# Kernel tuning notes

Measured on AMD Instinct MI355X. Metric: run time of the kernel, lower is better.

Reference implementation:

```python
import jax, jax.numpy as jnp
import numpy as np

NEG_SLOPE = 0.01  # torch nn.LeakyReLU default

N_NODES = 100000
N_EDGES = 1000000
D_FEAT = 64


def setup_inputs() -> dict:
    key = jax.random.key(0)
    ks = jax.random.split(key, 8)
    x = jax.random.normal(ks[0], (N_NODES, D_FEAT), dtype=jnp.float32)
    src = jax.random.randint(ks[1], (N_EDGES,), 0, N_NODES, dtype=jnp.int64 if jax.config.jax_enable_x64 else jnp.int32)
    dst = jax.random.randint(ks[2], (N_EDGES,), 0, N_NODES, dtype=jnp.int64 if jax.config.jax_enable_x64 else jnp.int32)
    s = 1.0 / np.sqrt(D_FEAT)
    W1 = jax.random.normal(ks[3], (D_FEAT, 64), dtype=jnp.float32) * s
    b1 = jnp.zeros((64,), dtype=jnp.float32)
    W2 = jax.random.normal(ks[4], (64, 64), dtype=jnp.float32) * s
    b2 = jnp.zeros((64,), dtype=jnp.float32)
    Wc = jax.random.normal(ks[5], (64, 2), dtype=jnp.float32) * s
    bc = jnp.zeros((2,), dtype=jnp.float32)
    return {"x": x, "src": src, "dst": dst, "W1": W1, "b1": b1,
            "W2": W2, "b2": b2, "Wc": Wc, "bc": bc}


def _graph_conv(x, src, dst, W, b, out_deg_isqrt, in_deg_isqrt, n_nodes):
    # DGL GraphConv, norm='both': h_v = ( sum_{u->v} x_u / sqrt(d_out(u)) ) / sqrt(d_in(v)) @ W + b
    # (in_feats <= out_feats here, so aggregate first then transform, matching DGL order)
    h = x * out_deg_isqrt[:, None]          # [N, d] scale by source out-degree
    msg = h[src]                            # [E, d] gather
    agg = jax.ops.segment_sum(msg, dst, num_segments=n_nodes)  # [N, d] scatter-add
    agg = agg * in_deg_isqrt[:, None]
    return agg @ W + b


def reference(x, src, dst, W1, b1, W2, b2, Wc, bc):
    n = x.shape[0]
    ones_e = jnp.ones(src.shape[0], dtype=x.dtype)
    out_deg = jnp.clip(jax.ops.segment_sum(ones_e, src, num_segments=n), 1.0)
    in_deg = jnp.clip(jax.ops.segment_sum(ones_e, dst, num_segments=n), 1.0)
    out_isqrt = out_deg ** -0.5
    in_isqrt = in_deg ** -0.5

    h = _graph_conv(x, src, dst, W1, b1, out_isqrt, in_isqrt, n)
    h = jax.nn.leaky_relu(h, NEG_SLOPE)
    h = _graph_conv(h, src, dst, W2, b2, out_isqrt, in_isqrt, n)
    h = jax.nn.leaky_relu(h, NEG_SLOPE)
    return h @ Wc + bc  # prediction=True -> linear classifier
```

## Files before the change

kernel.cpp:

```cpp
#include <hip/hip_runtime.h>


typedef __attribute__((ext_vector_type(8))) short short8;
typedef __attribute__((ext_vector_type(4))) float f32x4;

#define NPB 256
#define BSH 9
#define BW  512

__device__ __forceinline__ float b2f(unsigned short u) {
    return __uint_as_float(((unsigned int)u) << 16);
}
__device__ __forceinline__ unsigned short f2b(float f) {
    unsigned int i = __float_as_uint(f);
    unsigned int r = (i + 0x7FFFu + ((i >> 16) & 1u)) >> 16;
    return (unsigned short)r;
}

__global__ __launch_bounds__(256) void count_kernel(
    const int* __restrict__ src, const int* __restrict__ dst,
    int* __restrict__ cntD, int* __restrict__ cntS, int e, int chunk) {
    __shared__ int hD[256], hS[256];
    int t = threadIdx.x, pb = blockIdx.x;
    hD[t] = 0; hS[t] = 0;
    __syncthreads();
    int e0 = pb * chunk, e1 = min(e, e0 + chunk);
    for (int i = e0 + t; i < e1; i += 256) {
        atomicAdd(&hD[dst[i] >> BSH], 1);
        atomicAdd(&hS[src[i] >> BSH], 1);
    }
    __syncthreads();
    cntD[t * NPB + pb] = hD[t];
    cntS[t * NPB + pb] = hS[t];
}

__global__ __launch_bounds__(1024) void scanmat_kernel(int* __restrict__ cntD,
                                                       int* __restrict__ cntS) {
    int* a = (blockIdx.x == 0) ? cntD : cntS;
    __shared__ int s[1024];
    int t = threadIdx.x;
    int base = t * 64;
    int sum = 0;
    for (int j = 0; j < 64; j++) sum += a[base + j];
    s[t] = sum;
    __syncthreads();
    for (int d = 1; d < 1024; d <<= 1) {
        int x = (t >= d) ? s[t - d] : 0;
        __syncthreads();
        s[t] += x;
        __syncthreads();
    }
    int run = s[t] - sum;
    for (int j = 0; j < 64; j++) {
        int v = a[base + j];
        a[base + j] = run;
        run += v;
    }
}

__global__ __launch_bounds__(256) void part_kernel(
    const int* __restrict__ src, const int* __restrict__ dst,
    const int* __restrict__ cntD, const int* __restrict__ cntS,
    unsigned int* __restrict__ ebuf, unsigned short* __restrict__ sbuf,
    int e, int chunk) {
    __shared__ int cD[256], cS[256];
    int t = threadIdx.x, pb = blockIdx.x;
    cD[t] = cntD[t * NPB + pb];
    cS[t] = cntS[t * NPB + pb];
    __syncthreads();
    int e0 = pb * chunk, e1 = min(e, e0 + chunk);
    for (int i = e0 + t; i < e1; i += 256) {
        int s_ = src[i], d_ = dst[i];
        int pd = atomicAdd(&cD[d_ >> BSH], 1);
        ebuf[pd] = ((unsigned int)s_ << BSH) | (unsigned int)(d_ & (BW - 1));
        int ps_ = atomicAdd(&cS[s_ >> BSH], 1);
        sbuf[ps_] = (unsigned short)(s_ & (BW - 1));
    }
}

__global__ __launch_bounds__(256) void bucket_kernel(
    const unsigned int* __restrict__ ebuf, const unsigned short* __restrict__ sbuf,
    const int* __restrict__ cntD, const int* __restrict__ cntS,
    const float4* __restrict__ x4,
    int* __restrict__ row, float* __restrict__ ii, float* __restrict__ oi,
    int* __restrict__ csr, ushort4* __restrict__ xb, int n, int e) {
    __shared__ int cnt[BW], cur[BW], ocnt[BW], ps[256];
    __shared__ float ol[BW];
    int t = threadIdx.x, b = blockIdx.x;
    int v0 = b << BSH;
    int eb0 = cntD[b * NPB], eb1 = cntD[(b + 1) * NPB];
    int sb0 = cntS[b * NPB], sb1 = cntS[(b + 1) * NPB];
    cnt[t] = 0; cnt[t + 256] = 0;
    ocnt[t] = 0; ocnt[t + 256] = 0;
    __syncthreads();
    for (int i = eb0 + t; i < eb1; i += 256)
        atomicAdd(&cnt[ebuf[i] & (BW - 1)], 1);
    for (int i = sb0 + t; i < sb1; i += 256)
        atomicAdd(&ocnt[sbuf[i]], 1);
    __syncthreads();
    int c0 = cnt[2 * t], c1 = cnt[2 * t + 1];
    int pair = c0 + c1;
    ps[t] = pair;
    __syncthreads();
    for (int d = 1; d < 256; d <<= 1) {
        int x = (t >= d) ? ps[t - d] : 0;
        __syncthreads();
        ps[t] += x;
        __syncthreads();
    }
    int excl = ps[t] - pair;
    cur[2 * t] = excl;
    cur[2 * t + 1] = excl + c0;
    int v = v0 + 2 * t;
    if (v < n) {
        row[v] = eb0 + excl;
        ii[v] = rsqrtf((float)max(c0, 1));
    }
    if (v + 1 < n) {
        row[v + 1] = eb0 + excl + c0;
        ii[v + 1] = rsqrtf((float)max(c1, 1));
    }
    if (b == 0 && t == 0) row[n] = e;
    for (int j = t; j < BW; j += 256) {
        float o = rsqrtf((float)max(ocnt[j], 1));
        ol[j] = o;
        int vv = v0 + j;
        if (vv < n) oi[vv] = o;
    }
    __syncthreads();
    for (int i = eb0 + t; i < eb1; i += 256) {
        unsigned int p = ebuf[i];
        int r = atomicAdd(&cur[p & (BW - 1)], 1);
        csr[eb0 + r] = (int)(p >> BSH);
    }
    int nloc = min(BW, n - v0);
    for (int i = t; i < nloc * 16; i += 256) {
        int vl = i >> 4, q = i & 15;
        float s = ol[vl];
        float4 val = x4[(size_t)(v0 + vl) * 16 + q];
        xb[(size_t)(v0 + vl) * 16 + q] =
            make_ushort4(f2b(val.x * s), f2b(val.y * s), f2b(val.z * s), f2b(val.w * s));
    }
}

__global__ __launch_bounds__(256) void agg_kernel(
    const ushort4* __restrict__ featb, const int* __restrict__ row,
    const int* __restrict__ csr, float4* __restrict__ out4,
    int n, int nwaves) {
    int lane = threadIdx.x & 63;
    int q = lane >> 4, s = lane & 15;
    int wid = blockIdx.x * (blockDim.x >> 6) + (threadIdx.x >> 6);
    int ngroups = (n + 3) >> 2;

    for (int g = wid; g < ngroups; g += nwaves) {
        int v = (g << 2) + q;
        bool valid = v < n;
        int base = 0, cnt = 0;
        if (valid) { base = row[v]; cnt = row[v + 1] - base; }
        float4 a = make_float4(0.f, 0.f, 0.f, 0.f);
        int j = 0;
        for (; j + 7 < cnt; j += 8) {
            int u[8];
#pragma unroll
            for (int k = 0; k < 8; k++) u[k] = csr[base + j + k];
#pragma unroll
            for (int k = 0; k < 8; k++) {
                ushort4 f = featb[(size_t)u[k] * 16 + s];
                a.x += b2f(f.x); a.y += b2f(f.y); a.z += b2f(f.z); a.w += b2f(f.w);
            }
        }
        for (; j + 3 < cnt; j += 4) {
            int u[4];
#pragma unroll
            for (int k = 0; k < 4; k++) u[k] = csr[base + j + k];
#pragma unroll
            for (int k = 0; k < 4; k++) {
                ushort4 f = featb[(size_t)u[k] * 16 + s];
                a.x += b2f(f.x); a.y += b2f(f.y); a.z += b2f(f.z); a.w += b2f(f.w);
            }
        }
        for (; j < cnt; j++) {
            ushort4 f = featb[(size_t)csr[base + j] * 16 + s];
            a.x += b2f(f.x); a.y += b2f(f.y); a.z += b2f(f.z); a.w += b2f(f.w);
        }
        if (valid) out4[(size_t)v * 16 + s] = a;
    }
}

template <bool FINAL>
__global__ __launch_bounds__(256) void gemm_kernel(
    const float* __restrict__ agg, const float* __restrict__ ii,
    const float* __restrict__ oi,
    const float* __restrict__ W, const float* __restrict__ bias,
    const float* __restrict__ Wc, const float* __restrict__ bcl,
    void* __restrict__ out, int n, int nwaves) {
    int lane = threadIdx.x & 63;
    int m15 = lane & 15, quad = lane >> 4;
    int wid = blockIdx.x * (blockDim.x >> 6) + (threadIdx.x >> 6);
    int ngroups = (n + 15) >> 4;

    short8 bf[4][2];
#pragma unroll
    for (int nt = 0; nt < 4; nt++)
#pragma unroll
        for (int kk = 0; kk < 2; kk++)
#pragma unroll
            for (int j = 0; j < 8; j++)
                bf[nt][kk][j] = (short)f2b(W[(kk * 32 + quad * 8 + j) * 64 + nt * 16 + m15]);

    float bias_r[4];
#pragma unroll
    for (int nt = 0; nt < 4; nt++) bias_r[nt] = bias[nt * 16 + m15];

    float wc_r[4][2];
    float bc0 = 0.f, bc1 = 0.f;
    if constexpr (FINAL) {
#pragma unroll
        for (int nt = 0; nt < 4; nt++) {
            wc_r[nt][0] = Wc[(nt * 16 + m15) * 2];
            wc_r[nt][1] = Wc[(nt * 16 + m15) * 2 + 1];
        }
        bc0 = bcl[0];
        bc1 = bcl[1];
    }

    for (int g = wid; g < ngroups; g += nwaves) {
        int rbase = g << 4;
        int rm = min(rbase + m15, n - 1);
        float iiv = ii[rm];

        short8 af[2];
#pragma unroll
        for (int kk = 0; kk < 2; kk++) {
            const float4* p = (const float4*)(agg + (size_t)rm * 64 + kk * 32 + quad * 8);
            float4 x0 = p[0], x1 = p[1];
            af[kk][0] = (short)f2b(x0.x * iiv);
            af[kk][1] = (short)f2b(x0.y * iiv);
            af[kk][2] = (short)f2b(x0.z * iiv);
            af[kk][3] = (short)f2b(x0.w * iiv);
            af[kk][4] = (short)f2b(x1.x * iiv);
            af[kk][5] = (short)f2b(x1.y * iiv);
            af[kk][6] = (short)f2b(x1.z * iiv);
            af[kk][7] = (short)f2b(x1.w * iiv);
        }

        f32x4 acc[4];
#pragma unroll
        for (int nt = 0; nt < 4; nt++) {
            f32x4 z = {0.f, 0.f, 0.f, 0.f};
            z = __builtin_amdgcn_mfma_f32_16x16x32_bf16(af[0], bf[nt][0], z, 0, 0, 0);
            z = __builtin_amdgcn_mfma_f32_16x16x32_bf16(af[1], bf[nt][1], z, 0, 0, 0);
            acc[nt] = z;
        }

        if constexpr (!FINAL) {
#pragma unroll
            for (int r = 0; r < 4; r++) {
                int vr = rbase + quad * 4 + r;
                float os = (vr < n) ? oi[vr] : 0.f;
#pragma unroll
                for (int nt = 0; nt < 4; nt++) {
                    float o = acc[nt][r] + bias_r[nt];
                    o = (o > 0.f) ? o : 0.01f * o;
                    if (vr < n)
                        ((unsigned short*)out)[(size_t)vr * 64 + nt * 16 + m15] = f2b(o * os);
                }
            }
        } else {
#pragma unroll
            for (int r = 0; r < 4; r++) {
                float p0 = 0.f, p1 = 0.f;
#pragma unroll
                for (int nt = 0; nt < 4; nt++) {
                    float o = acc[nt][r] + bias_r[nt];
                    o = (o > 0.f) ? o : 0.01f * o;
                    p0 = fmaf(o, wc_r[nt][0], p0);
                    p1 = fmaf(o, wc_r[nt][1], p1);
                }
#pragma unroll
                for (int off = 1; off < 16; off <<= 1) {
                    p0 += __shfl_xor(p0, off);
                    p1 += __shfl_xor(p1, off);
                }
                int vr = rbase + quad * 4 + r;
                if (m15 == 0 && vr < n)
                    ((float2*)out)[vr] = make_float2(p0 + bc0, p1 + bc1);
            }
        }
    }
}

extern "C" void kernel_launch(void* const* d_in, const int* in_sizes, int n_in,
                              void* d_out, int out_size, void* d_ws, size_t ws_size,
                              hipStream_t stream) {
    const float* x  = (const float*)d_in[0];
    const int* src  = (const int*)d_in[1];
    const int* dst  = (const int*)d_in[2];
    const float* W1 = (const float*)d_in[3];
    const float* b1 = (const float*)d_in[4];
    const float* W2 = (const float*)d_in[5];
    const float* b2 = (const float*)d_in[6];
    const float* Wc = (const float*)d_in[7];
    const float* bc = (const float*)d_in[8];
    int n = in_sizes[0] / 64;
    int e = in_sizes[1];
    int total = n * 64;
    int nbuck = (n + BW - 1) >> BSH;

    char* ws = (char*)d_ws;
    size_t off = 0;
    auto take = [&](size_t bytes) -> char* {
        char* p = ws + off;
        off = (off + bytes + 255) & ~(size_t)255;
        return p;
    };
    int* cntD = (int*)take(256 * NPB * 4);
    int* cntS = (int*)take(256 * NPB * 4);
    unsigned int* ebuf = (unsigned int*)take((size_t)e * 4);
    unsigned short* sbuf = (unsigned short*)take((size_t)e * 2);
    int* row  = (int*)take((size_t)(n + 1) * 4);
    int* csr  = (int*)take((size_t)e * 4);
    float* oi = (float*)take((size_t)n * 4);
    float* ii = (float*)take((size_t)n * 4);
    unsigned short* xb  = (unsigned short*)take((size_t)total * 2);
    unsigned short* h1b = (unsigned short*)take((size_t)total * 2);
    float* aggbuf = (float*)take((size_t)total * 4);

    const int tb = 256;
    int chunk = (e + NPB - 1) / NPB;

    count_kernel<<<NPB, tb, 0, stream>>>(src, dst, cntD, cntS, e, chunk);
    scanmat_kernel<<<2, 1024, 0, stream>>>(cntD, cntS);
    part_kernel<<<NPB, tb, 0, stream>>>(src, dst, cntD, cntS, ebuf, sbuf, e, chunk);
    bucket_kernel<<<nbuck, tb, 0, stream>>>(ebuf, sbuf, cntD, cntS, (const float4*)x,
                                            row, ii, oi, csr, (ushort4*)xb, n, e);

    const int ablocks = 2048;
    const int awaves = ablocks * (tb / 64);
    const int gblocks = 512;
    const int gwaves = gblocks * (tb / 64);

    agg_kernel<<<ablocks, tb, 0, stream>>>((const ushort4*)xb, row, csr,
                                           (float4*)aggbuf, n, awaves);
    gemm_kernel<false><<<gblocks, tb, 0, stream>>>(aggbuf, ii, oi, W1, b1,
                                                   nullptr, nullptr, h1b, n, gwaves);
    agg_kernel<<<ablocks, tb, 0, stream>>>((const ushort4*)h1b, row, csr,
                                           (float4*)aggbuf, n, awaves);
    gemm_kernel<true><<<gblocks, tb, 0, stream>>>(aggbuf, ii, nullptr, W2, b2,
                                                  Wc, bc, d_out, n, gwaves);
}
```

Baseline: 232.4 us.

## Fuse neighbor aggregation and MFMA transform into one per-tile layer kernel

Each GCN layer becomes a single kernel. A block aggregates 128 destination nodes into padded LDS, synchronises, then runs the bf16 MFMA transform with bias, LeakyReLU and scaling straight from shared memory. This removes the fp32 aggregation buffer round-trip through global memory and two kernel launches. The cost is grid-stride balancing traded for fixed tiles of 782 blocks, roughly 35 KB of LDS per block, and W fragment setup repeated in every block.

```diff
diff --git a/kernel.cpp b/kernel.cpp
--- a/kernel.cpp
+++ b/kernel.cpp
@@ -7,6 +7,9 @@
 #define NPB 256
 #define BSH 9
 #define BW  512
+#define TSH 7
+#define TW  128
+#define STR 68
 
 __device__ __forceinline__ float b2f(unsigned short u) {
     return __uint_as_float(((unsigned int)u) << 16);
@@ -143,17 +146,48 @@
     }
 }
 
-__global__ __launch_bounds__(256) void agg_kernel(
+template <bool FINAL>
+__global__ __launch_bounds__(256) void layer_kernel(
     const ushort4* __restrict__ featb, const int* __restrict__ row,
-    const int* __restrict__ csr, float4* __restrict__ out4,
-    int n, int nwaves) {
-    int lane = threadIdx.x & 63;
+    const int* __restrict__ csr, const float* __restrict__ ii,
+    const float* __restrict__ oi,
+    const float* __restrict__ W, const float* __restrict__ bias,
+    const float* __restrict__ Wc, const float* __restrict__ bcl,
+    void* __restrict__ out, int n) {
+    __shared__ float accL[TW * STR];
+    int tid = threadIdx.x;
+    int lane = tid & 63;
+    int w = tid >> 6;
     int q = lane >> 4, s = lane & 15;
-    int wid = blockIdx.x * (blockDim.x >> 6) + (threadIdx.x >> 6);
-    int ngroups = (n + 3) >> 2;
-
-    for (int g = wid; g < ngroups; g += nwaves) {
-        int v = (g << 2) + q;
+    int m15 = s, quad = q;
+    int v0 = blockIdx.x << TSH;
+
+    short8 bf[4][2];
+#pragma unroll
+    for (int nt = 0; nt < 4; nt++)
+#pragma unroll
+        for (int kk = 0; kk < 2; kk++)
+#pragma unroll
+            for (int j = 0; j < 8; j++)
+                bf[nt][kk][j] = (short)f2b(W[(kk * 32 + quad * 8 + j) * 64 + nt * 16 + m15]);
+    float bias_r[4];
+#pragma unroll
+    for (int nt = 0; nt < 4; nt++) bias_r[nt] = bias[nt * 16 + m15];
+    float wc_r[4][2];
+    float bc0 = 0.f, bc1 = 0.f;
+    if constexpr (FINAL) {
+#pragma unroll
+        for (int nt = 0; nt < 4; nt++) {
+            wc_r[nt][0] = Wc[(nt * 16 + m15) * 2];
+            wc_r[nt][1] = Wc[(nt * 16 + m15) * 2 + 1];
+        }
+        bc0 = bcl[0];
+        bc1 = bcl[1];
+    }
+
+    for (int gl = w; gl < TW / 4; gl += 4) {
+        int vL = gl * 4 + q;
+        int v = v0 + vL;
         bool valid = v < n;
         int base = 0, cnt = 0;
         if (valid) { base = row[v]; cnt = row[v + 1] - base; }
@@ -183,56 +217,19 @@
             ushort4 f = featb[(size_t)csr[base + j] * 16 + s];
             a.x += b2f(f.x); a.y += b2f(f.y); a.z += b2f(f.z); a.w += b2f(f.w);
         }
-        if (valid) out4[(size_t)v * 16 + s] = a;
-    }
-}
-
-template <bool FINAL>
-__global__ __launch_bounds__(256) void gemm_kernel(
-    const float* __restrict__ agg, const float* __restrict__ ii,
-    const float* __restrict__ oi,
-    const float* __restrict__ W, const float* __restrict__ bias,
-    const float* __restrict__ Wc, const float* __restrict__ bcl,
-    void* __restrict__ out, int n, int nwaves) {
-    int lane = threadIdx.x & 63;
-    int m15 = lane & 15, quad = lane >> 4;
-    int wid = blockIdx.x * (blockDim.x >> 6) + (threadIdx.x >> 6);
-    int ngroups = (n + 15) >> 4;
-
-    short8 bf[4][2];
-#pragma unroll
-    for (int nt = 0; nt < 4; nt++)
-#pragma unroll
-        for (int kk = 0; kk < 2; kk++)
-#pragma unroll
-            for (int j = 0; j < 8; j++)
-                bf[nt][kk][j] = (short)f2b(W[(kk * 32 + quad * 8 + j) * 64 + nt * 16 + m15]);
-
-    float bias_r[4];
-#pragma unroll
-    for (int nt = 0; nt < 4; nt++) bias_r[nt] = bias[nt * 16 + m15];
-
-    float wc_r[4][2];
-    float bc0 = 0.f, bc1 = 0.f;
-    if constexpr (FINAL) {
-#pragma unroll
-        for (int nt = 0; nt < 4; nt++) {
-            wc_r[nt][0] = Wc[(nt * 16 + m15) * 2];
-            wc_r[nt][1] = Wc[(nt * 16 + m15) * 2 + 1];
-        }
-        bc0 = bcl[0];
-        bc1 = bcl[1];
-    }
-
-    for (int g = wid; g < ngroups; g += nwaves) {
-        int rbase = g << 4;
-        int rm = min(rbase + m15, n - 1);
-        float iiv = ii[rm];
+        *(float4*)&accL[vL * STR + s * 4] = a;
+    }
+    __syncthreads();
+
+    for (int t8 = w; t8 < TW / 16; t8 += 4) {
+        int rl = t8 * 16;
+        int rg = v0 + rl + m15;
+        float iiv = ii[min(rg, n - 1)];
 
         short8 af[2];
 #pragma unroll
         for (int kk = 0; kk < 2; kk++) {
-            const float4* p = (const float4*)(agg + (size_t)rm * 64 + kk * 32 + quad * 8);
+            const float4* p = (const float4*)&accL[(rl + m15) * STR + kk * 32 + quad * 8];
             float4 x0 = p[0], x1 = p[1];
             af[kk][0] = (short)f2b(x0.x * iiv);
             af[kk][1] = (short)f2b(x0.y * iiv);
@@ -256,7 +253,7 @@
         if constexpr (!FINAL) {
 #pragma unroll
             for (int r = 0; r < 4; r++) {
-                int vr = rbase + quad * 4 + r;
+                int vr = v0 + rl + quad * 4 + r;
                 float os = (vr < n) ? oi[vr] : 0.f;
 #pragma unroll
                 for (int nt = 0; nt < 4; nt++) {
@@ -282,7 +279,7 @@
                     p0 += __shfl_xor(p0, off);
                     p1 += __shfl_xor(p1, off);
                 }
-                int vr = rbase + quad * 4 + r;
+                int vr = v0 + rl + quad * 4 + r;
                 if (m15 == 0 && vr < n)
                     ((float2*)out)[vr] = make_float2(p0 + bc0, p1 + bc1);
             }
@@ -306,6 +303,7 @@
     int e = in_sizes[1];
     int total = n * 64;
     int nbuck = (n + BW - 1) >> BSH;
+    int ntile = (n + TW - 1) >> TSH;
 
     char* ws = (char*)d_ws;
     size_t off = 0;
@@ -324,7 +322,6 @@
     float* ii = (float*)take((size_t)n * 4);
     unsigned short* xb  = (unsigned short*)take((size_t)total * 2);
     unsigned short* h1b = (unsigned short*)take((size_t)total * 2);
-    float* aggbuf = (float*)take((size_t)total * 4);
 
     const int tb = 256;
     int chunk = (e + NPB - 1) / NPB;
@@ -335,17 +332,8 @@
     bucket_kernel<<<nbuck, tb, 0, stream>>>(ebuf, sbuf, cntD, cntS, (const float4*)x,
                                             row, ii, oi, csr, (ushort4*)xb, n, e);
 
-    const int ablocks = 2048;
-    const int awaves = ablocks * (tb / 64);
-    const int gblocks = 512;
-    const int gwaves = gblocks * (tb / 64);
-
-    agg_kernel<<<ablocks, tb, 0, stream>>>((const ushort4*)xb, row, csr,
-                                           (float4*)aggbuf, n, awaves);
-    gemm_kernel<false><<<gblocks, tb, 0, stream>>>(aggbuf, ii, oi, W1, b1,
-                                                   nullptr, nullptr, h1b, n, gwaves);
-    agg_kernel<<<ablocks, tb, 0, stream>>>((const ushort4*)h1b, row, csr,
-                                           (float4*)aggbuf, n, awaves);
-    gemm_kernel<true><<<gblocks, tb, 0, stream>>>(aggbuf, ii, nullptr, W2, b2,
-                                                  Wc, bc, d_out, n, gwaves);
-}
+    layer_kernel<false><<<ntile, tb, 0, stream>>>((const ushort4*)xb, row, csr, ii, oi,
+                                                  W1, b1, nullptr, nullptr, h1b, n);
+    layer_kernel<true><<<ntile, tb, 0, stream>>>((const ushort4*)h1b, row, csr, ii, oi,
+                                                 W2, b2, Wc, bc, d_out, n);
+}
```

Measured after the change: 303.5 us. 30.6% more time.

## Sort nodes by in-degree within buckets to balance aggregation waves

Applied to the files above, without the earlier changes.

The bucket kernel now counting-sorts the nodes of each 512-node bucket by in-degree (capped at 63) and writes a permutation. The aggregation kernel processes nodes in permuted order, so the four nodes sharing a wave have similar degrees and fewer lanes sit idle waiting on the longest neighbour list. This costs an extra indirection read per node, scattered output writes, and a serial 64-entry scan on one thread per bucket.

```diff
diff --git a/kernel.cpp b/kernel.cpp
--- a/kernel.cpp
+++ b/kernel.cpp
@@ -83,15 +83,19 @@
     const int* __restrict__ cntD, const int* __restrict__ cntS,
     const float4* __restrict__ x4,
     int* __restrict__ row, float* __restrict__ ii, float* __restrict__ oi,
-    int* __restrict__ csr, ushort4* __restrict__ xb, int n, int e) {
+    int* __restrict__ csr, ushort4* __restrict__ xb, int* __restrict__ perm,
+    int n, int e) {
     __shared__ int cnt[BW], cur[BW], ocnt[BW], ps[256];
     __shared__ float ol[BW];
+    __shared__ int dh[64];
     int t = threadIdx.x, b = blockIdx.x;
     int v0 = b << BSH;
     int eb0 = cntD[b * NPB], eb1 = cntD[(b + 1) * NPB];
     int sb0 = cntS[b * NPB], sb1 = cntS[(b + 1) * NPB];
+    int nloc = min(BW, n - v0);
     cnt[t] = 0; cnt[t + 256] = 0;
     ocnt[t] = 0; ocnt[t + 256] = 0;
+    if (t < 64) dh[t] = 0;
     __syncthreads();
     for (int i = eb0 + t; i < eb1; i += 256)
         atomicAdd(&cnt[ebuf[i] & (BW - 1)], 1);
@@ -127,13 +131,23 @@
         int vv = v0 + j;
         if (vv < n) oi[vv] = o;
     }
-    __syncthreads();
+    for (int j = t; j < nloc; j += 256)
+        atomicAdd(&dh[min(cnt[j], 63)], 1);
+    __syncthreads();
+    if (t == 0) {
+        int acc = 0;
+        for (int d = 0; d < 64; d++) { int x = dh[d]; dh[d] = acc; acc += x; }
+    }
+    __syncthreads();
+    for (int j = t; j < nloc; j += 256) {
+        int pos = atomicAdd(&dh[min(cnt[j], 63)], 1);
+        perm[v0 + pos] = v0 + j;
+    }
     for (int i = eb0 + t; i < eb1; i += 256) {
         unsigned int p = ebuf[i];
         int r = atomicAdd(&cur[p & (BW - 1)], 1);
         csr[eb0 + r] = (int)(p >> BSH);
     }
-    int nloc = min(BW, n - v0);
     for (int i = t; i < nloc * 16; i += 256) {
         int vl = i >> 4, q = i & 15;
         float s = ol[vl];
@@ -145,8 +159,8 @@
 
 __global__ __launch_bounds__(256) void agg_kernel(
     const ushort4* __restrict__ featb, const int* __restrict__ row,
-    const int* __restrict__ csr, float4* __restrict__ out4,
-    int n, int nwaves) {
+    const int* __restrict__ csr, const int* __restrict__ perm,
+    float4* __restrict__ out4, int n, int nwaves) {
     int lane = threadIdx.x & 63;
     int q = lane >> 4, s = lane & 15;
     int wid = blockIdx.x * (blockDim.x >> 6) + (threadIdx.x >> 6);
@@ -155,8 +169,12 @@
     for (int g = wid; g < ngroups; g += nwaves) {
         int v = (g << 2) + q;
         bool valid = v < n;
-        int base = 0, cnt = 0;
-        if (valid) { base = row[v]; cnt = row[v + 1] - base; }
+        int pv = 0, base = 0, cnt = 0;
+        if (valid) {
+            pv = perm[v];
+            base = row[pv];
+            cnt = row[pv + 1] - base;
+        }
         float4 a = make_float4(0.f, 0.f, 0.f, 0.f);
         int j = 0;
         for (; j + 7 < cnt; j += 8) {
@@ -183,7 +201,7 @@
             ushort4 f = featb[(size_t)csr[base + j] * 16 + s];
             a.x += b2f(f.x); a.y += b2f(f.y); a.z += b2f(f.z); a.w += b2f(f.w);
         }
-        if (valid) out4[(size_t)v * 16 + s] = a;
+        if (valid) out4[(size_t)pv * 16 + s] = a;
     }
 }
 
@@ -320,6 +338,7 @@
     unsigned short* sbuf = (unsigned short*)take((size_t)e * 2);
     int* row  = (int*)take((size_t)(n + 1) * 4);
     int* csr  = (int*)take((size_t)e * 4);
+    int* perm = (int*)take((size_t)n * 4);
     float* oi = (float*)take((size_t)n * 4);
     float* ii = (float*)take((size_t)n * 4);
     unsigned short* xb  = (unsigned short*)take((size_t)total * 2);
@@ -333,18 +352,18 @@
     scanmat_kernel<<<2, 1024, 0, stream>>>(cntD, cntS);
     part_kernel<<<NPB, tb, 0, stream>>>(src, dst, cntD, cntS, ebuf, sbuf, e, chunk);
     bucket_kernel<<<nbuck, tb, 0, stream>>>(ebuf, sbuf, cntD, cntS, (const float4*)x,
-                                            row, ii, oi, csr, (ushort4*)xb, n, e);
+                                            row, ii, oi, csr, (ushort4*)xb, perm, n, e);
 
     const int ablocks = 2048;
     const int awaves = ablocks * (tb / 64);
     const int gblocks = 512;
     const int gwaves = gblocks * (tb / 64);
 
-    agg_kernel<<<ablocks, tb, 0, stream>>>((const ushort4*)xb, row, csr,
+    agg_kernel<<<ablocks, tb, 0, stream>>>((const ushort4*)xb, row, csr, perm,
                                            (float4*)aggbuf, n, awaves);
     gemm_kernel<false><<<gblocks, tb, 0, stream>>>(aggbuf, ii, oi, W1, b1,
                                                    nullptr, nullptr, h1b, n, gwaves);
-    agg_kernel<<<ablocks, tb, 0, stream>>>((const ushort4*)h1b, row, csr,
+    agg_kernel<<<ablocks, tb, 0, stream>>>((const ushort4*)h1b, row, csr, perm,
                                            (float4*)aggbuf, n, awaves);
     gemm_kernel<true><<<gblocks, tb, 0, stream>>>(aggbuf, ii, nullptr, W2, b2,
                                                   Wc, bc, d_out, n, gwaves);
```

Result: slower. 243.7 us (+4.9%).

## Store aggregation output as scaled bf16 and widen gather to 16-byte loads

Applied to the files above, without the earlier changes.

The aggregation kernel now applies the in-degree scale and writes its result as bf16, so the intermediate buffer is half the size and the GEMM loads ready-made MFMA operands directly. The gather changes from 8-byte to 16-byte loads, with 8 lanes per node and 8 nodes per wave, and the 8-wide unrolled inner loop is removed. The aim is to cut intermediate write and read traffic and the number of gather transactions. In exchange there are fewer lanes per node row, more accumulator registers per lane, and a shallower unroll that may expose less memory-level parallelism.

```diff
diff --git a/kernel.cpp b/kernel.cpp
--- a/kernel.cpp
+++ b/kernel.cpp
@@ -144,52 +144,54 @@
 }
 
 __global__ __launch_bounds__(256) void agg_kernel(
-    const ushort4* __restrict__ featb, const int* __restrict__ row,
-    const int* __restrict__ csr, float4* __restrict__ out4,
-    int n, int nwaves) {
+    const short8* __restrict__ featb, const int* __restrict__ row,
+    const int* __restrict__ csr, const float* __restrict__ ii,
+    short8* __restrict__ outb, int n, int nwaves) {
     int lane = threadIdx.x & 63;
-    int q = lane >> 4, s = lane & 15;
+    int o = lane >> 3, s = lane & 7;
     int wid = blockIdx.x * (blockDim.x >> 6) + (threadIdx.x >> 6);
-    int ngroups = (n + 3) >> 2;
+    int ngroups = (n + 7) >> 3;
 
     for (int g = wid; g < ngroups; g += nwaves) {
-        int v = (g << 2) + q;
+        int v = (g << 3) + o;
         bool valid = v < n;
         int base = 0, cnt = 0;
         if (valid) { base = row[v]; cnt = row[v + 1] - base; }
-        float4 a = make_float4(0.f, 0.f, 0.f, 0.f);
+        float a[8];
+#pragma unroll
+        for (int k = 0; k < 8; k++) a[k] = 0.f;
         int j = 0;
-        for (; j + 7 < cnt; j += 8) {
-            int u[8];
-#pragma unroll
-            for (int k = 0; k < 8; k++) u[k] = csr[base + j + k];
-#pragma unroll
-            for (int k = 0; k < 8; k++) {
-                ushort4 f = featb[(size_t)u[k] * 16 + s];
-                a.x += b2f(f.x); a.y += b2f(f.y); a.z += b2f(f.z); a.w += b2f(f.w);
-            }
-        }
         for (; j + 3 < cnt; j += 4) {
             int u[4];
 #pragma unroll
             for (int k = 0; k < 4; k++) u[k] = csr[base + j + k];
 #pragma unroll
             for (int k = 0; k < 4; k++) {
-                ushort4 f = featb[(size_t)u[k] * 16 + s];
-                a.x += b2f(f.x); a.y += b2f(f.y); a.z += b2f(f.z); a.w += b2f(f.w);
+                short8 f = featb[(size_t)u[k] * 8 + s];
+#pragma unroll
+                for (int m = 0; m < 8; m++)
+                    a[m] += b2f((unsigned short)f[m]);
             }
         }
         for (; j < cnt; j++) {
-            ushort4 f = featb[(size_t)csr[base + j] * 16 + s];
-            a.x += b2f(f.x); a.y += b2f(f.y); a.z += b2f(f.z); a.w += b2f(f.w);
-        }
-        if (valid) out4[(size_t)v * 16 + s] = a;
+            short8 f = featb[(size_t)csr[base + j] * 8 + s];
+#pragma unroll
+            for (int m = 0; m < 8; m++)
+                a[m] += b2f((unsigned short)f[m]);
+        }
+        if (valid) {
+            float iiv = ii[v];
+            short8 r;
+#pragma unroll
+            for (int m = 0; m < 8; m++) r[m] = (short)f2b(a[m] * iiv);
+            outb[(size_t)v * 8 + s] = r;
+        }
     }
 }
 
 template <bool FINAL>
 __global__ __launch_bounds__(256) void gemm_kernel(
-    const float* __restrict__ agg, const float* __restrict__ ii,
+    const unsigned short* __restrict__ aggb,
     const float* __restrict__ oi,
     const float* __restrict__ W, const float* __restrict__ bias,
     const float* __restrict__ Wc, const float* __restrict__ bcl,
@@ -227,29 +229,17 @@
     for (int g = wid; g < ngroups; g += nwaves) {
         int rbase = g << 4;
         int rm = min(rbase + m15, n - 1);
-        float iiv = ii[rm];
-
-        short8 af[2];
-#pragma unroll
-        for (int kk = 0; kk < 2; kk++) {
-            const float4* p = (const float4*)(agg + (size_t)rm * 64 + kk * 32 + quad * 8);
-            float4 x0 = p[0], x1 = p[1];
-            af[kk][0] = (short)f2b(x0.x * iiv);
-            af[kk][1] = (short)f2b(x0.y * iiv);
-            af[kk][2] = (short)f2b(x0.z * iiv);
-            af[kk][3] = (short)f2b(x0.w * iiv);
-            af[kk][4] = (short)f2b(x1.x * iiv);
-            af[kk][5] = (short)f2b(x1.y * iiv);
-            af[kk][6] = (short)f2b(x1.z * iiv);
-            af[kk][7] = (short)f2b(x1.w * iiv);
-        }
+
+        const short8* arow = (const short8*)(aggb + (size_t)rm * 64);
+        short8 af0 = arow[quad];
+        short8 af1 = arow[4 + quad];
 
         f32x4 acc[4];
 #pragma unroll
         for (int nt = 0; nt < 4; nt++) {
             f32x4 z = {0.f, 0.f, 0.f, 0.f};
-            z = __builtin_amdgcn_mfma_f32_16x16x32_bf16(af[0], bf[nt][0], z, 0, 0, 0);
-            z = __builtin_amdgcn_mfma_f32_16x16x32_bf16(af[1], bf[nt][1], z, 0, 0, 0);
+            z = __builtin_amdgcn_mfma_f32_16x16x32_bf16(af0, bf[nt][0], z, 0, 0, 0);
+            z = __builtin_amdgcn_mfma_f32_16x16x32_bf16(af1, bf[nt][1], z, 0, 0, 0);
             acc[nt] = z;
         }
 
@@ -324,7 +314,7 @@
     float* ii = (float*)take((size_t)n * 4);
     unsigned short* xb  = (unsigned short*)take((size_t)total * 2);
     unsigned short* h1b = (unsigned short*)take((size_t)total * 2);
-    float* aggbuf = (float*)take((size_t)total * 4);
+    unsigned short* aggb = (unsigned short*)take((size_t)total * 2);
 
     const int tb = 256;
     int chunk = (e + NPB - 1) / NPB;
@@ -340,12 +330,12 @@
     const int gblocks = 512;
     const int gwaves = gblocks * (tb / 64);
 
-    agg_kernel<<<ablocks, tb, 0, stream>>>((const ushort4*)xb, row, csr,
-                                           (float4*)aggbuf, n, awaves);
-    gemm_kernel<false><<<gblocks, tb, 0, stream>>>(aggbuf, ii, oi, W1, b1,
+    agg_kernel<<<ablocks, tb, 0, stream>>>((const short8*)xb, row, csr, ii,
+                                           (short8*)aggb, n, awaves);
+    gemm_kernel<false><<<gblocks, tb, 0, stream>>>(aggb, oi, W1, b1,
                                                    nullptr, nullptr, h1b, n, gwaves);
-    agg_kernel<<<ablocks, tb, 0, stream>>>((const ushort4*)h1b, row, csr,
-                                           (float4*)aggbuf, n, awaves);
-    gemm_kernel<true><<<gblocks, tb, 0, stream>>>(aggbuf, ii, nullptr, W2, b2,
+    agg_kernel<<<ablocks, tb, 0, stream>>>((const short8*)h1b, row, csr, ii,
+                                           (short8*)aggb, n, awaves);
+    gemm_kernel<true><<<gblocks, tb, 0, stream>>>(aggb, oi, W2, b2,
                                                   Wc, bc, d_out, n, gwaves);
 }
```

Result: faster. 219.0 us (-5.8%).
